# Optimization experiments

Measured on AMD Instinct MI355X. Metric: run time of the kernel, lower is better.

Reference implementation:

```python
import jax, jax.numpy as jnp
import numpy as np

N_NODES = 500000
N_EDGES = 2000000
F_IN = 117
HIDDEN = 128
NLAYERS = 3


def setup_inputs() -> dict:
    key = jax.random.key(0)
    ks = jax.random.split(key, 8)
    x = jax.random.normal(ks[0], (N_NODES, F_IN), dtype=jnp.float32)
    edge_src = jax.random.randint(ks[1], (N_EDGES,), 0, N_NODES, dtype=jnp.int32)
    edge_dst = jax.random.randint(ks[2], (N_EDGES,), 0, N_NODES, dtype=jnp.int32)
    W_in = jax.random.normal(ks[3], (F_IN, HIDDEN), dtype=jnp.float32) * 0.05
    b_in = jax.random.normal(ks[4], (HIDDEN,), dtype=jnp.float32) * 0.05
    W_self = jax.random.normal(ks[5], (NLAYERS, HIDDEN, HIDDEN), dtype=jnp.float32) * 0.05
    W_neigh = jax.random.normal(ks[6], (NLAYERS, HIDDEN, HIDDEN), dtype=jnp.float32) * 0.05
    b_layers = jax.random.normal(ks[7], (NLAYERS, HIDDEN), dtype=jnp.float32) * 0.05
    return {"x": x, "edge_src": edge_src, "edge_dst": edge_dst,
            "W_in": W_in, "b_in": b_in,
            "W_self": W_self, "W_neigh": W_neigh, "b_layers": b_layers}


def reference(x, edge_src, edge_dst, W_in, b_in, W_self, W_neigh, b_layers):
    # Input projection: Linear(117 -> 128) + Tanh
    h = jnp.tanh(x @ W_in + b_in)  # [N, H]
    N = h.shape[0]

    # In-degree per destination node (static; zero-degree nodes get zero mean)
    deg = jax.ops.segment_sum(jnp.ones_like(edge_dst, dtype=h.dtype), edge_dst,
                              num_segments=N)  # [N]
    inv_deg = (1.0 / jnp.maximum(deg, 1.0))[:, None]  # [N, 1]

    # Stacked SAGEConv('mean') layers: relu(h @ W_self + mean_neigh @ W_neigh + b)
    for l in range(NLAYERS):
        neigh_sum = jax.ops.segment_sum(h[edge_src], edge_dst, num_segments=N)  # [N, H]
        h_neigh = neigh_sum * inv_deg
        h = jax.nn.relu(h @ W_self[l] + h_neigh @ W_neigh[l] + b_layers[l])
    return h
```

## Files before the change

### kernel.cpp

```cpp
#include <hip/hip_runtime.h>

#define N_NODES 500000
#define N_EDGES 2000000
#define F_IN 117
#define H 128
#define NLAYERS 3

#define SCAN_E 2048
#define NB_SCAN ((N_NODES + SCAN_E - 1) / SCAN_E)
#define NBUCKET ((N_NODES + 511) >> 9)
#define FILL_CHUNK 8192
#define NB_FILL ((N_EDGES + FILL_CHUNK - 1) / FILL_CHUNK)

typedef __attribute__((ext_vector_type(8))) short short8v;
typedef __attribute__((ext_vector_type(4))) float f32x4;

__device__ __forceinline__ unsigned short f2bf(float x) {
    unsigned u = __builtin_bit_cast(unsigned, x);
    u += 0x7FFFu + ((u >> 16) & 1u);
    return (unsigned short)(u >> 16);
}
__device__ __forceinline__ float bf2f(unsigned short s) {
    unsigned u = ((unsigned)s) << 16;
    return __builtin_bit_cast(float, u);
}
__device__ __forceinline__ float fast_tanh(float x) {
    float e = __builtin_amdgcn_exp2f(x * 2.885390081777927f);
    return 1.0f - 2.0f * __builtin_amdgcn_rcpf(e + 1.0f);
}

__global__ void prep_w_kernel(const float* __restrict__ Wself,
                              const float* __restrict__ Wneigh,
                              const float* __restrict__ Win,
                              short* __restrict__ Wfrag,
                              short* __restrict__ WfragIn) {
    const int tid = blockIdx.x * 256 + threadIdx.x;
    const int total_cmb = NLAYERS * 64 * 64;
    if (tid < total_cmb) {
        const int lane = tid & 63;
        const int fi   = (tid >> 6) & 63;
        const int l    = tid >> 12;
        const int ks = fi & 7, ct = (fi >> 3) & 3, wc = fi >> 5;
        const int c = wc * 64 + ct * 16 + (lane & 15);
        const int kbase = ks * 32 + (lane >> 4) * 8;
        short8v out;
        #pragma unroll
        for (int j = 0; j < 8; ++j) {
            int k = kbase + j;
            float v = (k < 128) ? Wself [(size_t)l * H * H + k * H + c]
                                : Wneigh[(size_t)l * H * H + (k - 128) * H + c];
            out[j] = (short)f2bf(v);
        }
        *(short8v*)(Wfrag + (size_t)tid * 8) = out;
    } else if (tid < total_cmb + 32 * 64) {
        const int t2 = tid - total_cmb;
        const int lane = t2 & 63;
        const int fi   = t2 >> 6;
        const int ks = fi & 3, ct = (fi >> 2) & 3, wc = fi >> 4;
        const int c = wc * 64 + ct * 16 + (lane & 15);
        const int kbase = ks * 32 + (lane >> 4) * 8;
        short8v out;
        #pragma unroll
        for (int j = 0; j < 8; ++j) {
            int k = kbase + j;
            out[j] = (k < F_IN) ? (short)f2bf(Win[(size_t)k * H + c]) : (short)0;
        }
        *(short8v*)(WfragIn + (size_t)t2 * 8) = out;
    }
}

__global__ __launch_bounds__(512, 2) void proj_mfma(const short* __restrict__ WfragIn,
                                                    const float* __restrict__ bias,
                                                    const float* __restrict__ x,
                                                    unsigned short* __restrict__ hb) {
    const int wave = threadIdx.x >> 6;
    const int lane = threadIdx.x & 63;
    const int wc   = wave & 1;

    short8v Bf[4][4];
    #pragma unroll
    for (int ct = 0; ct < 4; ++ct)
        #pragma unroll
        for (int ks = 0; ks < 4; ++ks)
            Bf[ct][ks] = ((const short8v*)WfragIn)[(size_t)(((wc * 4 + ct) * 4 + ks) * 64 + lane)];

    float bs[4];
    #pragma unroll
    for (int ct = 0; ct < 4; ++ct) bs[ct] = bias[wc * 64 + ct * 16 + (lane & 15)];

    const int cbase = (lane >> 4) * 8;
    const int ntasks = (N_NODES / 16) * 2;
    for (int task = blockIdx.x * 8 + wave; task < ntasks; task += gridDim.x * 8) {
        const int r0  = (task >> 1) * 16;
        const int row = r0 + (lane & 15);
        const float* xr = x + (size_t)row * F_IN;

        short8v Af[4];
        #pragma unroll
        for (int ks = 0; ks < 4; ++ks) {
            const int k0 = ks * 32 + cbase;
            short8v a;
            if (row == N_NODES - 1 && k0 + 7 >= F_IN) {
                #pragma unroll
                for (int j = 0; j < 8; ++j) {
                    int k = k0 + j;
                    a[j] = (k < F_IN) ? (short)f2bf(xr[k]) : (short)0;
                }
            } else {
                #pragma unroll
                for (int j = 0; j < 8; ++j) a[j] = (short)f2bf(xr[k0 + j]);
            }
            Af[ks] = a;
        }

        f32x4 acc[4];
        #pragma unroll
        for (int ct = 0; ct < 4; ++ct) acc[ct] = (f32x4){0.f, 0.f, 0.f, 0.f};
        #pragma unroll
        for (int ks = 0; ks < 4; ++ks)
            #pragma unroll
            for (int ct = 0; ct < 4; ++ct)
                acc[ct] = __builtin_amdgcn_mfma_f32_16x16x32_bf16(Af[ks], Bf[ct][ks], acc[ct], 0, 0, 0);

        #pragma unroll
        for (int ct = 0; ct < 4; ++ct) {
            const int col = wc * 64 + ct * 16 + (lane & 15);
            #pragma unroll
            for (int q = 0; q < 4; ++q) {
                float v = fast_tanh(acc[ct][q] + bs[ct]);
                hb[(size_t)(r0 + (lane >> 4) * 4 + q) * H + col] = f2bf(v);
            }
        }
    }
}

__global__ void zero_int_kernel(int* __restrict__ p, int n) {
    int i = blockIdx.x * blockDim.x + threadIdx.x;
    if (i < n) p[i] = 0;
}

__global__ void hist_kernel(const int* __restrict__ dst, int* __restrict__ cnt) {
    int e = blockIdx.x * blockDim.x + threadIdx.x;
    if (e < N_EDGES) atomicAdd(&cnt[dst[e]], 1);
}

__global__ __launch_bounds__(256) void scan_reduce_kernel(const int* __restrict__ cnt,
                                                          int* __restrict__ bsums) {
    __shared__ int s[256];
    const int base = blockIdx.x * SCAN_E;
    int sum = 0;
    for (int i = threadIdx.x; i < SCAN_E; i += 256) {
        int idx = base + i;
        sum += (idx < N_NODES) ? cnt[idx] : 0;
    }
    s[threadIdx.x] = sum;
    __syncthreads();
    for (int off = 128; off > 0; off >>= 1) {
        if (threadIdx.x < off) s[threadIdx.x] += s[threadIdx.x + off];
        __syncthreads();
    }
    if (threadIdx.x == 0) bsums[blockIdx.x] = s[0];
}

__global__ void scan_bsums_kernel(int* __restrict__ bsums) {
    __shared__ int s[256];
    const int tid = threadIdx.x;
    int v = (tid < NB_SCAN) ? bsums[tid] : 0;
    s[tid] = v;
    __syncthreads();
    for (int off = 1; off < 256; off <<= 1) {
        int add = (tid >= off) ? s[tid - off] : 0;
        __syncthreads();
        s[tid] += add;
        __syncthreads();
    }
    if (tid < NB_SCAN) bsums[tid] = s[tid] - v;
}

__global__ __launch_bounds__(256) void scan_final_kernel(const int* __restrict__ cnt,
                                                         const int* __restrict__ bsums,
                                                         int* __restrict__ start,
                                                         float* __restrict__ inv,
                                                         int* __restrict__ bcur) {
    __shared__ int tsum[256];
    const int tid = threadIdx.x;
    const int base = blockIdx.x * SCAN_E + tid * 8;
    int c[8];
    int s = 0;
    #pragma unroll
    for (int k = 0; k < 8; ++k) {
        int idx = base + k;
        c[k] = (idx < N_NODES) ? cnt[idx] : 0;
        s += c[k];
    }
    tsum[tid] = s;
    __syncthreads();
    for (int off = 1; off < 256; off <<= 1) {
        int add = (tid >= off) ? tsum[tid - off] : 0;
        __syncthreads();
        tsum[tid] += add;
        __syncthreads();
    }
    int off0 = bsums[blockIdx.x] + tsum[tid] - s;
    #pragma unroll
    for (int k = 0; k < 8; ++k) {
        int idx = base + k;
        if (idx < N_NODES) {
            start[idx] = off0;
            inv[idx]   = 1.0f / fmaxf((float)c[k], 1.0f);
            if ((idx & 511) == 0) bcur[idx >> 9] = off0;
            off0 += c[k];
        }
    }
}

__global__ __launch_bounds__(256) void bin_fill_kernel(const int* __restrict__ src,
                                                       const int* __restrict__ dst,
                                                       int* __restrict__ bcur,
                                                       int2* __restrict__ pairs) {
    __shared__ int2 ep[FILL_CHUNK];
    __shared__ int  hist[NBUCKET];
    const int t  = threadIdx.x;
    const int e0 = blockIdx.x * FILL_CHUNK;
    const int n  = min(FILL_CHUNK, N_EDGES - e0);

    for (int i = t; i < NBUCKET; i += 256) hist[i] = 0;
    __syncthreads();
    for (int i = t; i < n; i += 256) {
        int s = src[e0 + i], d = dst[e0 + i];
        ep[i] = make_int2(s, d);
        atomicAdd(&hist[d >> 9], 1);
    }
    __syncthreads();
    for (int i = t; i < NBUCKET; i += 256) {
        int c = hist[i];
        hist[i] = c ? atomicAdd(&bcur[i], c) : 0;
    }
    __syncthreads();
    for (int i = t; i < n; i += 256) {
        int2 p = ep[i];
        int pos = atomicAdd(&hist[p.y >> 9], 1);
        pairs[pos] = p;
    }
}

__global__ __launch_bounds__(256) void bucket_scatter_kernel(const int* __restrict__ start,
                                                             const int2* __restrict__ pairs,
                                                             int* __restrict__ srcs) {
    __shared__ int cur[512];
    const int b   = blockIdx.x;
    const int nb0 = b << 9;
    const int nend = min(nb0 + 512, N_NODES);
    const int t = threadIdx.x;
    for (int i = t; i < nend - nb0; i += 256) cur[i] = start[nb0 + i];
    __syncthreads();
    const int ebeg = start[nb0];
    const int eend = (nend < N_NODES) ? start[nend] : N_EDGES;
    for (int i = ebeg + t; i < eend; i += 256) {
        int2 p = pairs[i];
        int pos = atomicAdd(&cur[p.y - nb0], 1);
        srcs[pos] = p.x;
    }
}

__global__ __launch_bounds__(256) void gather_kernel(const int* __restrict__ start,
                                                     const int* __restrict__ cnt,
                                                     const int* __restrict__ srcs,
                                                     const float* __restrict__ inv,
                                                     const unsigned short* __restrict__ hb,
                                                     unsigned short* __restrict__ nsb) {
    const int idx  = blockIdx.x * 256 + threadIdx.x;
    const int node = idx >> 4;
    if (node >= N_NODES) return;
    const int f = (idx & 15) * 8;
    const int st = start[node];
    const int c  = cnt[node];
    float a[8];
    #pragma unroll
    for (int i = 0; i < 8; ++i) a[i] = 0.f;
    int j = 0;
    for (; j + 4 <= c; j += 4) {
        const int s0 = srcs[st + j + 0];
        const int s1 = srcs[st + j + 1];
        const int s2 = srcs[st + j + 2];
        const int s3 = srcs[st + j + 3];
        const short8v v0 = *(const short8v*)(hb + (size_t)s0 * H + f);
        const short8v v1 = *(const short8v*)(hb + (size_t)s1 * H + f);
        const short8v v2 = *(const short8v*)(hb + (size_t)s2 * H + f);
        const short8v v3 = *(const short8v*)(hb + (size_t)s3 * H + f);
        #pragma unroll
        for (int i = 0; i < 8; ++i)
            a[i] += (bf2f((unsigned short)v0[i]) + bf2f((unsigned short)v1[i]))
                  + (bf2f((unsigned short)v2[i]) + bf2f((unsigned short)v3[i]));
    }
    if (j + 2 <= c) {
        const int s0 = srcs[st + j + 0];
        const int s1 = srcs[st + j + 1];
        const short8v v0 = *(const short8v*)(hb + (size_t)s0 * H + f);
        const short8v v1 = *(const short8v*)(hb + (size_t)s1 * H + f);
        #pragma unroll
        for (int i = 0; i < 8; ++i)
            a[i] += bf2f((unsigned short)v0[i]) + bf2f((unsigned short)v1[i]);
        j += 2;
    }
    if (j < c) {
        const int s0 = srcs[st + j];
        const short8v v0 = *(const short8v*)(hb + (size_t)s0 * H + f);
        #pragma unroll
        for (int i = 0; i < 8; ++i) a[i] += bf2f((unsigned short)v0[i]);
    }
    const float iv = inv[node];
    short8v o;
    #pragma unroll
    for (int i = 0; i < 8; ++i) o[i] = (short)f2bf(a[i] * iv);
    *(short8v*)(nsb + (size_t)node * H + f) = o;
}

__global__ __launch_bounds__(512, 2) void combine_mfma(const short* __restrict__ Wfrag,
                                                       const float* __restrict__ bias,
                                                       const unsigned short* __restrict__ hb,
                                                       const unsigned short* __restrict__ nsb,
                                                       unsigned short* __restrict__ outb,
                                                       float* __restrict__ outf,
                                                       int last) {
    const int wave = threadIdx.x >> 6;
    const int lane = threadIdx.x & 63;
    const int wc   = wave & 1;

    short8v Bf[4][8];
    #pragma unroll
    for (int ct = 0; ct < 4; ++ct)
        #pragma unroll
        for (int ks = 0; ks < 8; ++ks)
            Bf[ct][ks] = ((const short8v*)Wfrag)[(size_t)(((wc * 4 + ct) * 8 + ks) * 64 + lane)];

    float bs[4];
    #pragma unroll
    for (int ct = 0; ct < 4; ++ct) bs[ct] = bias[wc * 64 + ct * 16 + (lane & 15)];

    const int ntasks = (N_NODES / 16) * 2;
    for (int task = blockIdx.x * 8 + wave; task < ntasks; task += gridDim.x * 8) {
        const int r0 = (task >> 1) * 16;
        const unsigned short* arow = hb  + (size_t)(r0 + (lane & 15)) * H + (lane >> 4) * 8;
        const unsigned short* nrow = nsb + (size_t)(r0 + (lane & 15)) * H + (lane >> 4) * 8;
        short8v Af[8];
        #pragma unroll
        for (int ks = 0; ks < 4; ++ks) Af[ks]     = *(const short8v*)(arow + ks * 32);
        #pragma unroll
        for (int ks = 0; ks < 4; ++ks) Af[4 + ks] = *(const short8v*)(nrow + ks * 32);

        f32x4 acc[4];
        #pragma unroll
        for (int ct = 0; ct < 4; ++ct) acc[ct] = (f32x4){0.f, 0.f, 0.f, 0.f};
        #pragma unroll
        for (int ks = 0; ks < 8; ++ks)
            #pragma unroll
            for (int ct = 0; ct < 4; ++ct)
                acc[ct] = __builtin_amdgcn_mfma_f32_16x16x32_bf16(Af[ks], Bf[ct][ks], acc[ct], 0, 0, 0);

        if (!last) {
            #pragma unroll
            for (int ct = 0; ct < 4; ++ct) {
                const int col = wc * 64 + ct * 16 + (lane & 15);
                #pragma unroll
                for (int q = 0; q < 4; ++q) {
                    float v = fmaxf(acc[ct][q] + bs[ct], 0.f);
                    outb[(size_t)(r0 + (lane >> 4) * 4 + q) * H + col] = f2bf(v);
                }
            }
        } else {
            #pragma unroll
            for (int ct = 0; ct < 4; ++ct) {
                const int col = wc * 64 + ct * 16 + (lane & 15);
                #pragma unroll
                for (int q = 0; q < 4; ++q) {
                    float v = fmaxf(acc[ct][q] + bs[ct], 0.f);
                    outf[(size_t)(r0 + (lane >> 4) * 4 + q) * H + col] = v;
                }
            }
        }
    }
}

extern "C" void kernel_launch(void* const* d_in, const int* in_sizes, int n_in,
                              void* d_out, int out_size, void* d_ws, size_t ws_size,
                              hipStream_t stream) {
    const float* x        = (const float*)d_in[0];
    const int*   edge_src = (const int*)d_in[1];
    const int*   edge_dst = (const int*)d_in[2];
    const float* W_in     = (const float*)d_in[3];
    const float* b_in     = (const float*)d_in[4];
    const float* W_self   = (const float*)d_in[5];
    const float* W_neigh  = (const float*)d_in[6];
    const float* b_layers = (const float*)d_in[7];

    unsigned short* h0  = (unsigned short*)d_ws;
    unsigned short* nsb = h0 + (size_t)N_NODES * H;
    int*   cnt    = (int*)(nsb + (size_t)N_NODES * H);
    int*   start  = cnt + N_NODES;
    float* inv    = (float*)(start + N_NODES);
    int*   srcs   = (int*)(inv + N_NODES);
    int*   bsums  = srcs + N_EDGES;
    short* Wfrag  = (short*)(bsums + 256);
    short* WfragIn = Wfrag + (size_t)NLAYERS * 64 * 64 * 8;
    int*   bcur   = (int*)(WfragIn + 32 * 64 * 8);
    int2*  pairs  = (int2*)nsb;
    unsigned short* h1 = (unsigned short*)d_out;

    prep_w_kernel<<<(NLAYERS * 64 * 64 + 32 * 64 + 255) / 256, 256, 0, stream>>>(
        W_self, W_neigh, W_in, Wfrag, WfragIn);

    zero_int_kernel<<<(N_NODES + 255) / 256, 256, 0, stream>>>(cnt, N_NODES);
    hist_kernel<<<(N_EDGES + 255) / 256, 256, 0, stream>>>(edge_dst, cnt);
    scan_reduce_kernel<<<NB_SCAN, 256, 0, stream>>>(cnt, bsums);
    scan_bsums_kernel<<<1, 256, 0, stream>>>(bsums);
    scan_final_kernel<<<NB_SCAN, 256, 0, stream>>>(cnt, bsums, start, inv, bcur);
    bin_fill_kernel<<<NB_FILL, 256, 0, stream>>>(edge_src, edge_dst, bcur, pairs);
    bucket_scatter_kernel<<<NBUCKET, 256, 0, stream>>>(start, pairs, srcs);

    proj_mfma<<<1024, 512, 0, stream>>>(WfragIn, b_in, x, h0);

    const int gather_grid = (N_NODES * 16 + 255) / 256;
    gather_kernel<<<gather_grid, 256, 0, stream>>>(start, cnt, srcs, inv, h0, nsb);
    combine_mfma<<<1024, 512, 0, stream>>>(Wfrag + 0 * 64 * 64 * 8, b_layers + 0 * H,
                                           h0, nsb, h1, nullptr, 0);
    gather_kernel<<<gather_grid, 256, 0, stream>>>(start, cnt, srcs, inv, h1, nsb);
    combine_mfma<<<1024, 512, 0, stream>>>(Wfrag + 1 * 64 * 64 * 8, b_layers + 1 * H,
                                           h1, nsb, h0, nullptr, 0);
    gather_kernel<<<gather_grid, 256, 0, stream>>>(start, cnt, srcs, inv, h0, nsb);
    combine_mfma<<<1024, 512, 0, stream>>>(Wfrag + 2 * 64 * 64 * 8, b_layers + 2 * H,
                                           h0, nsb, nullptr, (float*)d_out, 1);
}
```

Measured before the change: 917.4 us.

## Stage MFMA epilogues through LDS for coalesced stores; vectorize x loads; deepen gather

```diff
diff --git a/kernel.cpp b/kernel.cpp
--- a/kernel.cpp
+++ b/kernel.cpp
@@ -14,6 +14,7 @@
 
 typedef __attribute__((ext_vector_type(8))) short short8v;
 typedef __attribute__((ext_vector_type(4))) float f32x4;
+typedef float __attribute__((ext_vector_type(4), aligned(4))) f32x4u;
 
 __device__ __forceinline__ unsigned short f2bf(float x) {
     unsigned u = __builtin_bit_cast(unsigned, x);
@@ -73,9 +74,11 @@
                                                     const float* __restrict__ bias,
                                                     const float* __restrict__ x,
                                                     unsigned short* __restrict__ hb) {
+    __shared__ __align__(16) char eplds[8][16 * 72 * 2];
     const int wave = threadIdx.x >> 6;
     const int lane = threadIdx.x & 63;
     const int wc   = wave & 1;
+    char* myl = &eplds[wave][0];
 
     short8v Bf[4][4];
     #pragma unroll
@@ -107,8 +110,12 @@
                     a[j] = (k < F_IN) ? (short)f2bf(xr[k]) : (short)0;
                 }
             } else {
-                #pragma unroll
-                for (int j = 0; j < 8; ++j) a[j] = (short)f2bf(xr[k0 + j]);
+                const f32x4u p0 = *(const f32x4u*)(xr + k0);
+                const f32x4u p1 = *(const f32x4u*)(xr + k0 + 4);
+                a[0] = (short)f2bf(p0[0]); a[1] = (short)f2bf(p0[1]);
+                a[2] = (short)f2bf(p0[2]); a[3] = (short)f2bf(p0[3]);
+                a[4] = (short)f2bf(p1[0]); a[5] = (short)f2bf(p1[1]);
+                a[6] = (short)f2bf(p1[2]); a[7] = (short)f2bf(p1[3]);
             }
             Af[ks] = a;
         }
@@ -122,15 +129,23 @@
             for (int ct = 0; ct < 4; ++ct)
                 acc[ct] = __builtin_amdgcn_mfma_f32_16x16x32_bf16(Af[ks], Bf[ct][ks], acc[ct], 0, 0, 0);
 
-        #pragma unroll
-        for (int ct = 0; ct < 4; ++ct) {
-            const int col = wc * 64 + ct * 16 + (lane & 15);
-            #pragma unroll
-            for (int q = 0; q < 4; ++q) {
-                float v = fast_tanh(acc[ct][q] + bs[ct]);
-                hb[(size_t)(r0 + (lane >> 4) * 4 + q) * H + col] = f2bf(v);
-            }
-        }
+        unsigned short* lh = (unsigned short*)myl;
+        #pragma unroll
+        for (int ct = 0; ct < 4; ++ct)
+            #pragma unroll
+            for (int q = 0; q < 4; ++q)
+                lh[((lane >> 4) * 4 + q) * 72 + ct * 16 + (lane & 15)] =
+                    f2bf(fast_tanh(acc[ct][q] + bs[ct]));
+        asm volatile("s_waitcnt lgkmcnt(0)" ::: "memory");
+        __builtin_amdgcn_sched_barrier(0);
+        #pragma unroll
+        for (int i = 0; i < 2; ++i) {
+            const int g = i * 64 + lane;
+            const int rw = g >> 3, seg = g & 7;
+            uint4 val = *(const uint4*)(myl + rw * 144 + seg * 16);
+            *(uint4*)(hb + (size_t)(r0 + rw) * H + wc * 64 + seg * 8) = val;
+        }
+        asm volatile("" ::: "memory");
     }
 }
 
@@ -279,33 +294,41 @@
     #pragma unroll
     for (int i = 0; i < 8; ++i) a[i] = 0.f;
     int j = 0;
-    for (; j + 4 <= c; j += 4) {
-        const int s0 = srcs[st + j + 0];
-        const int s1 = srcs[st + j + 1];
-        const int s2 = srcs[st + j + 2];
-        const int s3 = srcs[st + j + 3];
-        const short8v v0 = *(const short8v*)(hb + (size_t)s0 * H + f);
-        const short8v v1 = *(const short8v*)(hb + (size_t)s1 * H + f);
-        const short8v v2 = *(const short8v*)(hb + (size_t)s2 * H + f);
-        const short8v v3 = *(const short8v*)(hb + (size_t)s3 * H + f);
+    for (; j + 8 <= c; j += 8) {
+        short8v v[8];
+        #pragma unroll
+        for (int u = 0; u < 8; ++u)
+            v[u] = *(const short8v*)(hb + (size_t)srcs[st + j + u] * H + f);
+        #pragma unroll
+        for (int i = 0; i < 8; ++i) {
+            float s0 = (bf2f((unsigned short)v[0][i]) + bf2f((unsigned short)v[1][i]))
+                     + (bf2f((unsigned short)v[2][i]) + bf2f((unsigned short)v[3][i]));
+            float s1 = (bf2f((unsigned short)v[4][i]) + bf2f((unsigned short)v[5][i]))
+                     + (bf2f((unsigned short)v[6][i]) + bf2f((unsigned short)v[7][i]));
+            a[i] += s0 + s1;
+        }
+    }
+    if (j + 4 <= c) {
+        short8v v[4];
+        #pragma unroll
+        for (int u = 0; u < 4; ++u)
+            v[u] = *(const short8v*)(hb + (size_t)srcs[st + j + u] * H + f);
         #pragma unroll
         for (int i = 0; i < 8; ++i)
-            a[i] += (bf2f((unsigned short)v0[i]) + bf2f((unsigned short)v1[i]))
-                  + (bf2f((unsigned short)v2[i]) + bf2f((unsigned short)v3[i]));
+            a[i] += (bf2f((unsigned short)v[0][i]) + bf2f((unsigned short)v[1][i]))
+                  + (bf2f((unsigned short)v[2][i]) + bf2f((unsigned short)v[3][i]));
+        j += 4;
     }
     if (j + 2 <= c) {
-        const int s0 = srcs[st + j + 0];
-        const int s1 = srcs[st + j + 1];
-        const short8v v0 = *(const short8v*)(hb + (size_t)s0 * H + f);
-        const short8v v1 = *(const short8v*)(hb + (size_t)s1 * H + f);
+        const short8v v0 = *(const short8v*)(hb + (size_t)srcs[st + j + 0] * H + f);
+        const short8v v1 = *(const short8v*)(hb + (size_t)srcs[st + j + 1] * H + f);
         #pragma unroll
         for (int i = 0; i < 8; ++i)
             a[i] += bf2f((unsigned short)v0[i]) + bf2f((unsigned short)v1[i]);
         j += 2;
     }
     if (j < c) {
-        const int s0 = srcs[st + j];
-        const short8v v0 = *(const short8v*)(hb + (size_t)s0 * H + f);
+        const short8v v0 = *(const short8v*)(hb + (size_t)srcs[st + j] * H + f);
         #pragma unroll
         for (int i = 0; i < 8; ++i) a[i] += bf2f((unsigned short)v0[i]);
     }
@@ -323,9 +346,11 @@
                                                        unsigned short* __restrict__ outb,
                                                        float* __restrict__ outf,
                                                        int last) {
+    __shared__ __align__(16) char eplds[8][16 * 68 * 4];
     const int wave = threadIdx.x >> 6;
     const int lane = threadIdx.x & 63;
     const int wc   = wave & 1;
+    char* myl = &eplds[wave][0];
 
     short8v Bf[4][8];
     #pragma unroll
@@ -359,26 +384,41 @@
                 acc[ct] = __builtin_amdgcn_mfma_f32_16x16x32_bf16(Af[ks], Bf[ct][ks], acc[ct], 0, 0, 0);
 
         if (!last) {
-            #pragma unroll
-            for (int ct = 0; ct < 4; ++ct) {
-                const int col = wc * 64 + ct * 16 + (lane & 15);
+            unsigned short* lh = (unsigned short*)myl;
+            #pragma unroll
+            for (int ct = 0; ct < 4; ++ct)
                 #pragma unroll
-                for (int q = 0; q < 4; ++q) {
-                    float v = fmaxf(acc[ct][q] + bs[ct], 0.f);
-                    outb[(size_t)(r0 + (lane >> 4) * 4 + q) * H + col] = f2bf(v);
-                }
+                for (int q = 0; q < 4; ++q)
+                    lh[((lane >> 4) * 4 + q) * 72 + ct * 16 + (lane & 15)] =
+                        f2bf(fmaxf(acc[ct][q] + bs[ct], 0.f));
+            asm volatile("s_waitcnt lgkmcnt(0)" ::: "memory");
+            __builtin_amdgcn_sched_barrier(0);
+            #pragma unroll
+            for (int i = 0; i < 2; ++i) {
+                const int g = i * 64 + lane;
+                const int rw = g >> 3, seg = g & 7;
+                uint4 val = *(const uint4*)(myl + rw * 144 + seg * 16);
+                *(uint4*)(outb + (size_t)(r0 + rw) * H + wc * 64 + seg * 8) = val;
             }
         } else {
-            #pragma unroll
-            for (int ct = 0; ct < 4; ++ct) {
-                const int col = wc * 64 + ct * 16 + (lane & 15);
+            float* lf = (float*)myl;
+            #pragma unroll
+            for (int ct = 0; ct < 4; ++ct)
                 #pragma unroll
-                for (int q = 0; q < 4; ++q) {
-                    float v = fmaxf(acc[ct][q] + bs[ct], 0.f);
-                    outf[(size_t)(r0 + (lane >> 4) * 4 + q) * H + col] = v;
-                }
+                for (int q = 0; q < 4; ++q)
+                    lf[((lane >> 4) * 4 + q) * 68 + ct * 16 + (lane & 15)] =
+                        fmaxf(acc[ct][q] + bs[ct], 0.f);
+            asm volatile("s_waitcnt lgkmcnt(0)" ::: "memory");
+            __builtin_amdgcn_sched_barrier(0);
+            #pragma unroll
+            for (int i = 0; i < 4; ++i) {
+                const int g = i * 64 + lane;
+                const int rw = g >> 4, seg = g & 15;
+                float4 val = *(const float4*)(lf + rw * 68 + seg * 4);
+                *(float4*)(outf + (size_t)(r0 + rw) * H + wc * 64 + seg * 4) = val;
             }
         }
+        asm volatile("" ::: "memory");
     }
 }
 
```

Result: slower. 969.5 us (+5.7%).
